# Kernel optimization log

Measured on AMD Instinct MI355X. Metric: run time of the kernel, lower is better.

The kernel has to match this reference:

```python
import jax, jax.numpy as jnp
import numpy as np

B, F = 64, 2048

def setup_inputs() -> dict:
    key = jax.random.key(0)
    k1, k2, k3, k4, k5 = jax.random.split(key, 5)
    scale = 1.0 / np.sqrt(F)
    return {
        "x": jax.random.normal(k1, (B, F), dtype=jnp.float32),
        "feature_mask": jax.random.randint(k2, (B, F), 0, 2, dtype=jnp.int32),
        "Wq": jax.random.normal(k3, (F, F), dtype=jnp.float32) * scale,
        "Wk": jax.random.normal(k4, (F, F), dtype=jnp.float32) * scale,
        "Wv": jax.random.normal(k5, (F, F), dtype=jnp.float32) * scale,
    }

def reference(x, feature_mask, Wq, Wk, Wv):
    # nn.Linear(bias=False): y = x @ W.T
    q = x @ Wq.T  # (B, F)
    k = x @ Wk.T
    v = x @ Wv.T
    # outer-product scores: (B, F, F) = q[:, :, None] * k[:, None, :]
    scores = q[:, :, None] * k[:, None, :]
    # mask broadcast over query dim (unsqueeze(1) in torch)
    scores = jnp.where(feature_mask[:, None, :] == 0, -1e9, scores)
    attn = jax.nn.softmax(scores, axis=-1)  # (B, F, F)
    attended = jnp.einsum("bfg,bg->bf", attn, v)  # (B, F)
    return attended
```

## Files before the change

### kernel.cpp

```cpp
#include <hip/hip_runtime.h>
#include <hip/hip_bf16.h>

#define B 64
#define F 2048
#define BN 32
#define BK 32
#define KSPLIT 4
#define KCHUNK (F / KSPLIT)
#define NITER (KCHUNK / BK)
#define LDSW 40
#define GS 4
#define NSEG 2
#define SEGG 1024

typedef __attribute__((ext_vector_type(8))) short bf16x8;
typedef __attribute__((ext_vector_type(4))) float f32x4;

#define PART_FLOATS (KSPLIT * 3 * B * F)
#define KVC_FLOATS (B * 2 * F)
#define QS_FLOATS (B * F)

#if __has_builtin(__builtin_amdgcn_exp2f)
#define EXP2(x) __builtin_amdgcn_exp2f(x)
#else
#define EXP2(x) exp2f(x)
#endif

__device__ __forceinline__ void split2(float f0, float f1, int& hi, int& lo) {
  union { float f; unsigned u; } a, b;
  a.f = f0; b.f = f1;
  union { unsigned u; float f; } ha, hb;
  ha.u = a.u & 0xFFFF0000u;
  hb.u = b.u & 0xFFFF0000u;
  union { float f; unsigned u; } la, lb;
  la.f = f0 - ha.f;
  lb.f = f1 - hb.f;
  hi = (int)__builtin_amdgcn_perm(b.u, a.u, 0x07060302u);
  lo = (int)__builtin_amdgcn_perm(lb.u, la.u, 0x07060302u);
}

__global__ __launch_bounds__(256) void qkv_gemm_kernel(
    const float* __restrict__ x, const float* __restrict__ Wq,
    const float* __restrict__ Wk, const float* __restrict__ Wv,
    float* __restrict__ part) {
  __shared__ __align__(16) short xs_hi[2][B][LDSW];
  __shared__ __align__(16) short xs_lo[2][B][LDSW];
  __shared__ __align__(16) short ws_hi[2][BN][LDSW];
  __shared__ __align__(16) short ws_lo[2][BN][LDSW];

  const int tid  = threadIdx.x;
  const int f0   = blockIdx.x * BN;
  const int kb   = blockIdx.y;
  const int mat  = blockIdx.z;
  const float* W = (mat == 0) ? Wq : (mat == 1) ? Wk : Wv;

  const int lrow = tid >> 2;
  const int lc0  = (tid & 3) << 3;
  const int wrow = tid >> 3;
  const int wc0  = (tid & 7) << 2;

  const int wave = tid >> 6;
  const int lane = tid & 63;
  const int l15  = lane & 15;
  const int quad = lane >> 4;

  const float* xg = x + lrow * F + kb * KCHUNK + lc0;
  const float* wg = W + (f0 + wrow) * F + kb * KCHUNK + wc0;

  f32x4 acc[2];
#pragma unroll
  for (int i = 0; i < 2; ++i) acc[i] = (f32x4){0.f, 0.f, 0.f, 0.f};

  float4 px[2][2], pw[2];
  px[0][0] = *(const float4*)(xg);
  px[0][1] = *(const float4*)(xg + 4);
  pw[0]    = *(const float4*)(wg);

#pragma unroll
  for (int it = 0; it < NITER; ++it) {
    const int cur = it & 1, nxt = cur ^ 1;
    if (it + 1 < NITER) {
      const float* xp = xg + (it + 1) * BK;
      px[nxt][0] = *(const float4*)(xp);
      px[nxt][1] = *(const float4*)(xp + 4);
      pw[nxt]    = *(const float4*)(wg + (it + 1) * BK);
    }
    int4 xh, xl;
    int2 wh, wl;
    split2(px[cur][0].x, px[cur][0].y, xh.x, xl.x);
    split2(px[cur][0].z, px[cur][0].w, xh.y, xl.y);
    split2(px[cur][1].x, px[cur][1].y, xh.z, xl.z);
    split2(px[cur][1].z, px[cur][1].w, xh.w, xl.w);
    split2(pw[cur].x, pw[cur].y, wh.x, wl.x);
    split2(pw[cur].z, pw[cur].w, wh.y, wl.y);
    *(int4*)&xs_hi[cur][lrow][lc0] = xh;
    *(int4*)&xs_lo[cur][lrow][lc0] = xl;
    *(int2*)&ws_hi[cur][wrow][wc0] = wh;
    *(int2*)&ws_lo[cur][wrow][wc0] = wl;
    __syncthreads();

    bf16x8 a_hi = *(const bf16x8*)&xs_hi[cur][(wave << 4) + l15][quad << 3];
    bf16x8 a_lo = *(const bf16x8*)&xs_lo[cur][(wave << 4) + l15][quad << 3];
#pragma unroll
    for (int nt = 0; nt < 2; ++nt) {
      bf16x8 b_hi = *(const bf16x8*)&ws_hi[cur][(nt << 4) + l15][quad << 3];
      bf16x8 b_lo = *(const bf16x8*)&ws_lo[cur][(nt << 4) + l15][quad << 3];
      acc[nt] = __builtin_amdgcn_mfma_f32_16x16x32_bf16(a_hi, b_hi, acc[nt], 0, 0, 0);
      acc[nt] = __builtin_amdgcn_mfma_f32_16x16x32_bf16(a_hi, b_lo, acc[nt], 0, 0, 0);
      acc[nt] = __builtin_amdgcn_mfma_f32_16x16x32_bf16(a_lo, b_hi, acc[nt], 0, 0, 0);
    }
  }

  float* outp = part + (size_t)(kb * 3 + mat) * B * F;
#pragma unroll
  for (int nt = 0; nt < 2; ++nt) {
    int f = f0 + (nt << 4) + l15;
#pragma unroll
    for (int r = 0; r < 4; ++r) {
      int brow = (wave << 4) + (quad << 2) + r;
      outp[brow * F + f] = acc[nt][r];
    }
  }
}

__global__ __launch_bounds__(256) void prep_kernel(
    const float* __restrict__ part, const int* __restrict__ mask,
    float* __restrict__ kvc, float* __restrict__ qs,
    float* __restrict__ vsum2, float* __restrict__ kmax2,
    float* __restrict__ kmin2, int* __restrict__ cnt2) {
  __shared__ int cnt;
  __shared__ float svs[4], smx[4], smn[4];

  const int b    = blockIdx.x;
  const int seg  = blockIdx.y;
  const int tid  = threadIdx.x;
  const int wave = tid >> 6;
  const int lane = tid & 63;

  if (tid == 0) cnt = 0;
  __syncthreads();

  const int g0 = seg * SEGG + (tid << 2);
  float4 qq = {0.f, 0.f, 0.f, 0.f};
  float4 kq = {0.f, 0.f, 0.f, 0.f}, vq = {0.f, 0.f, 0.f, 0.f};
#pragma unroll
  for (int p = 0; p < KSPLIT; ++p) {
    const float4 qp = *(const float4*)&part[((p * 3 + 0) * B + b) * F + g0];
    const float4 kp = *(const float4*)&part[((p * 3 + 1) * B + b) * F + g0];
    const float4 vp = *(const float4*)&part[((p * 3 + 2) * B + b) * F + g0];
    qq.x += qp.x; qq.y += qp.y; qq.z += qp.z; qq.w += qp.w;
    kq.x += kp.x; kq.y += kp.y; kq.z += kp.z; kq.w += kp.w;
    vq.x += vp.x; vq.y += vp.y; vq.z += vp.z; vq.w += vp.w;
  }
  *(float4*)&qs[b * F + g0] = qq;
  float vs = (vq.x + vq.y) + (vq.z + vq.w);

  const int4 m4 = *(const int4*)&mask[b * F + g0];
  const float kk[4] = {kq.x, kq.y, kq.z, kq.w};
  const float vv[4] = {vq.x, vq.y, vq.z, vq.w};
  const bool  act[4] = {m4.x != 0, m4.y != 0, m4.z != 0, m4.w != 0};

  unsigned long long bal[4];
  int tot = 0;
#pragma unroll
  for (int j = 0; j < 4; ++j) {
    bal[j] = __ballot(act[j]);
    tot += __popcll(bal[j]);
  }
  int base = 0;
  if (lane == 0) base = atomicAdd(&cnt, tot);
  base = __shfl(base, 0);

  float* kvb = kvc + (size_t)b * 2 * F + seg * 2 * SEGG;
  const unsigned long long ltm = (1ull << lane) - 1ull;
  float kmx = -3.4e38f, kmn = 3.4e38f;
  int off = base;
#pragma unroll
  for (int j = 0; j < 4; ++j) {
    if (act[j]) {
      int pos = off + __popcll(bal[j] & ltm);
      *(float2*)&kvb[2 * pos] = (float2){kk[j], vv[j]};
      kmx = fmaxf(kmx, kk[j]);
      kmn = fminf(kmn, kk[j]);
    }
    off += __popcll(bal[j]);
  }

#pragma unroll
  for (int o = 32; o > 0; o >>= 1) {
    vs += __shfl_xor(vs, o);
    kmx = fmaxf(kmx, __shfl_xor(kmx, o));
    kmn = fminf(kmn, __shfl_xor(kmn, o));
  }
  if (lane == 0) { svs[wave] = vs; smx[wave] = kmx; smn[wave] = kmn; }
  __syncthreads();
  if (tid == 0) {
    vsum2[b * NSEG + seg] = svs[0] + svs[1] + svs[2] + svs[3];
    kmax2[b * NSEG + seg] = fmaxf(fmaxf(smx[0], smx[1]), fmaxf(smx[2], smx[3]));
    kmin2[b * NSEG + seg] = fminf(fminf(smn[0], smn[1]), fminf(smn[2], smn[3]));
    cnt2[b * NSEG + seg]  = cnt;
  }
}

__global__ __launch_bounds__(1024, 8) void attn_kernel(
    const float* __restrict__ qs, const float* __restrict__ kvc,
    const float* __restrict__ vsum2, const float* __restrict__ kmax2,
    const float* __restrict__ kmin2, const int* __restrict__ cnt2,
    float* __restrict__ out) {
  __shared__ float rn[GS][256];
  __shared__ float rd[GS][256];

  const int b     = blockIdx.x;
  const int tid   = threadIdx.x;
  const int fl    = tid & 255;
  const int slice = __builtin_amdgcn_readfirstlane(tid >> 8);
  const int fi    = blockIdx.y * 256 + fl;

  const float s = qs[b * F + fi];

  int cnts[NSEG];
  float km = -3.4e38f, kn = 3.4e38f;
  int ntot = 0;
  float vstot = 0.f;
#pragma unroll
  for (int g2 = 0; g2 < NSEG; ++g2) {
    cnts[g2] = cnt2[b * NSEG + g2];
    ntot += cnts[g2];
    km = fmaxf(km, kmax2[b * NSEG + g2]);
    kn = fminf(kn, kmin2[b * NSEG + g2]);
    vstot += vsum2[b * NSEG + g2];
  }

  const float L2E = 1.44269504088896f;
  const float se  = s * L2E;
  const float nm2 = -se * ((s >= 0.f) ? km : kn);

  float n0 = 0.f, n1 = 0.f, n2 = 0.f, n3 = 0.f;
  float d0 = 0.f, d1 = 0.f, d2 = 0.f, d3 = 0.f;
  const float* kvbase = kvc + (size_t)b * 2 * F;
#pragma unroll
  for (int seg = 0; seg < NSEG; ++seg) {
    const int cnt   = cnts[seg];
    const int quads = cnt >> 1;
    const int q0 = (slice * quads) / GS;
    const int q1 = ((slice + 1) * quads) / GS;
    const float4* bp = (const float4*)(kvbase + seg * 2 * SEGG);
    int q = q0;
    for (; q + 4 <= q1; q += 4) {
      float4 p0 = bp[q];
      float4 p1 = bp[q + 1];
      float4 p2 = bp[q + 2];
      float4 p3 = bp[q + 3];
      float e0 = EXP2(fmaf(se, p0.x, nm2));
      float e1 = EXP2(fmaf(se, p0.z, nm2));
      float e2 = EXP2(fmaf(se, p1.x, nm2));
      float e3 = EXP2(fmaf(se, p1.z, nm2));
      float e4 = EXP2(fmaf(se, p2.x, nm2));
      float e5 = EXP2(fmaf(se, p2.z, nm2));
      float e6 = EXP2(fmaf(se, p3.x, nm2));
      float e7 = EXP2(fmaf(se, p3.z, nm2));
      n0 = fmaf(e0, p0.y, n0); d0 += e0;
      n1 = fmaf(e1, p0.w, n1); d1 += e1;
      n2 = fmaf(e2, p1.y, n2); d2 += e2;
      n3 = fmaf(e3, p1.w, n3); d3 += e3;
      n0 = fmaf(e4, p2.y, n0); d0 += e4;
      n1 = fmaf(e5, p2.w, n1); d1 += e5;
      n2 = fmaf(e6, p3.y, n2); d2 += e6;
      n3 = fmaf(e7, p3.w, n3); d3 += e7;
    }
    for (; q < q1; ++q) {
      float4 p0 = bp[q];
      float e0 = EXP2(fmaf(se, p0.x, nm2));
      float e1 = EXP2(fmaf(se, p0.z, nm2));
      n0 = fmaf(e0, p0.y, n0); d0 += e0;
      n1 = fmaf(e1, p0.w, n1); d1 += e1;
    }
    if ((slice == GS - 1) && (cnt & 1)) {
      float2 p = *(const float2*)(kvbase + seg * 2 * SEGG + 2 * (cnt - 1));
      float e = EXP2(fmaf(se, p.x, nm2));
      n2 = fmaf(e, p.y, n2); d2 += e;
    }
  }
  rn[slice][fl] = (n0 + n1) + (n2 + n3);
  rd[slice][fl] = (d0 + d1) + (d2 + d3);
  __syncthreads();
  if (slice == 0) {
    float N = (rn[0][fl] + rn[1][fl]) + (rn[2][fl] + rn[3][fl]);
    float D = (rd[0][fl] + rd[1][fl]) + (rd[2][fl] + rd[3][fl]);
    out[b * F + fi] = (ntot > 0) ? (N / D) : (vstot * (1.0f / (float)F));
  }
}

extern "C" void kernel_launch(void* const* d_in, const int* in_sizes, int n_in,
                              void* d_out, int out_size, void* d_ws, size_t ws_size,
                              hipStream_t stream) {
  const float* x  = (const float*)d_in[0];
  const int* mask = (const int*)d_in[1];
  const float* Wq = (const float*)d_in[2];
  const float* Wk = (const float*)d_in[3];
  const float* Wv = (const float*)d_in[4];
  float* out = (float*)d_out;

  float* part  = (float*)d_ws;
  float* kvc   = part + PART_FLOATS;
  float* qs    = kvc + KVC_FLOATS;
  float* vsum2 = qs + QS_FLOATS;
  float* kmx2  = vsum2 + B * NSEG;
  float* kmn2  = kmx2 + B * NSEG;
  int*   cnt2  = (int*)(kmn2 + B * NSEG);

  dim3 gg(F / BN, KSPLIT, 3);
  qkv_gemm_kernel<<<gg, 256, 0, stream>>>(x, Wq, Wk, Wv, part);
  dim3 gp(B, NSEG);
  prep_kernel<<<gp, 256, 0, stream>>>(part, mask, kvc, qs, vsum2, kmx2, kmn2, cnt2);
  dim3 ga(B, F / 256);
  attn_kernel<<<ga, 1024, 0, stream>>>(qs, kvc, vsum2, kmx2, kmn2, cnt2, out);
}
```

Baseline: 122.6 us.

## Fuse prep into attention kernel, compacting masked keys into LDS per block

Removes the separate prep kernel. Each attention block now reduces the split-K partials for its own q values and for the full k/v row, then compacts unmasked (k,v) pairs into shared memory via ballot and atomics. The block also computes max/min of k and the sum of v. The inner softmax loop reads from LDS instead of global memory, and one launch plus the global intermediates go away. In exchange, each of the 8 blocks per batch row redoes the k/v reduction and compaction, and each block uses about 16KB of extra LDS, which may lower occupancy.

```diff
diff --git a/kernel.cpp b/kernel.cpp
--- a/kernel.cpp
+++ b/kernel.cpp
@@ -10,15 +10,11 @@
 #define NITER (KCHUNK / BK)
 #define LDSW 40
 #define GS 4
-#define NSEG 2
-#define SEGG 1024
 
 typedef __attribute__((ext_vector_type(8))) short bf16x8;
 typedef __attribute__((ext_vector_type(4))) float f32x4;
 
 #define PART_FLOATS (KSPLIT * 3 * B * F)
-#define KVC_FLOATS (B * 2 * F)
-#define QS_FLOATS (B * F)
 
 #if __has_builtin(__builtin_amdgcn_exp2f)
 #define EXP2(x) __builtin_amdgcn_exp2f(x)
@@ -123,112 +119,79 @@
   }
 }
 
-__global__ __launch_bounds__(256) void prep_kernel(
+__global__ __launch_bounds__(1024, 8) void attn_kernel(
     const float* __restrict__ part, const int* __restrict__ mask,
-    float* __restrict__ kvc, float* __restrict__ qs,
-    float* __restrict__ vsum2, float* __restrict__ kmax2,
-    float* __restrict__ kmin2, int* __restrict__ cnt2) {
-  __shared__ int cnt;
-  __shared__ float svs[4], smx[4], smn[4];
-
-  const int b    = blockIdx.x;
-  const int seg  = blockIdx.y;
-  const int tid  = threadIdx.x;
-  const int wave = tid >> 6;
-  const int lane = tid & 63;
-
-  if (tid == 0) cnt = 0;
-  __syncthreads();
-
-  const int g0 = seg * SEGG + (tid << 2);
-  float4 qq = {0.f, 0.f, 0.f, 0.f};
-  float4 kq = {0.f, 0.f, 0.f, 0.f}, vq = {0.f, 0.f, 0.f, 0.f};
-#pragma unroll
-  for (int p = 0; p < KSPLIT; ++p) {
-    const float4 qp = *(const float4*)&part[((p * 3 + 0) * B + b) * F + g0];
-    const float4 kp = *(const float4*)&part[((p * 3 + 1) * B + b) * F + g0];
-    const float4 vp = *(const float4*)&part[((p * 3 + 2) * B + b) * F + g0];
-    qq.x += qp.x; qq.y += qp.y; qq.z += qp.z; qq.w += qp.w;
-    kq.x += kp.x; kq.y += kp.y; kq.z += kp.z; kq.w += kp.w;
-    vq.x += vp.x; vq.y += vp.y; vq.z += vp.z; vq.w += vp.w;
-  }
-  *(float4*)&qs[b * F + g0] = qq;
-  float vs = (vq.x + vq.y) + (vq.z + vq.w);
-
-  const int4 m4 = *(const int4*)&mask[b * F + g0];
-  const float kk[4] = {kq.x, kq.y, kq.z, kq.w};
-  const float vv[4] = {vq.x, vq.y, vq.z, vq.w};
-  const bool  act[4] = {m4.x != 0, m4.y != 0, m4.z != 0, m4.w != 0};
-
-  unsigned long long bal[4];
-  int tot = 0;
-#pragma unroll
-  for (int j = 0; j < 4; ++j) {
-    bal[j] = __ballot(act[j]);
-    tot += __popcll(bal[j]);
-  }
-  int base = 0;
-  if (lane == 0) base = atomicAdd(&cnt, tot);
-  base = __shfl(base, 0);
-
-  float* kvb = kvc + (size_t)b * 2 * F + seg * 2 * SEGG;
-  const unsigned long long ltm = (1ull << lane) - 1ull;
-  float kmx = -3.4e38f, kmn = 3.4e38f;
-  int off = base;
-#pragma unroll
-  for (int j = 0; j < 4; ++j) {
-    if (act[j]) {
-      int pos = off + __popcll(bal[j] & ltm);
-      *(float2*)&kvb[2 * pos] = (float2){kk[j], vv[j]};
-      kmx = fmaxf(kmx, kk[j]);
-      kmn = fminf(kmn, kk[j]);
-    }
-    off += __popcll(bal[j]);
-  }
-
-#pragma unroll
-  for (int o = 32; o > 0; o >>= 1) {
-    vs += __shfl_xor(vs, o);
-    kmx = fmaxf(kmx, __shfl_xor(kmx, o));
-    kmn = fminf(kmn, __shfl_xor(kmn, o));
-  }
-  if (lane == 0) { svs[wave] = vs; smx[wave] = kmx; smn[wave] = kmn; }
-  __syncthreads();
-  if (tid == 0) {
-    vsum2[b * NSEG + seg] = svs[0] + svs[1] + svs[2] + svs[3];
-    kmax2[b * NSEG + seg] = fmaxf(fmaxf(smx[0], smx[1]), fmaxf(smx[2], smx[3]));
-    kmin2[b * NSEG + seg] = fminf(fminf(smn[0], smn[1]), fminf(smn[2], smn[3]));
-    cnt2[b * NSEG + seg]  = cnt;
-  }
-}
-
-__global__ __launch_bounds__(1024, 8) void attn_kernel(
-    const float* __restrict__ qs, const float* __restrict__ kvc,
-    const float* __restrict__ vsum2, const float* __restrict__ kmax2,
-    const float* __restrict__ kmin2, const int* __restrict__ cnt2,
     float* __restrict__ out) {
+  __shared__ __align__(16) float kvs[2 * F];
   __shared__ float rn[GS][256];
   __shared__ float rd[GS][256];
+  __shared__ float swv[16], swm[16], swn[16];
+  __shared__ int scnt;
 
   const int b     = blockIdx.x;
   const int tid   = threadIdx.x;
   const int fl    = tid & 255;
   const int slice = __builtin_amdgcn_readfirstlane(tid >> 8);
   const int fi    = blockIdx.y * 256 + fl;
-
-  const float s = qs[b * F + fi];
-
-  int cnts[NSEG];
-  float km = -3.4e38f, kn = 3.4e38f;
-  int ntot = 0;
-  float vstot = 0.f;
-#pragma unroll
-  for (int g2 = 0; g2 < NSEG; ++g2) {
-    cnts[g2] = cnt2[b * NSEG + g2];
-    ntot += cnts[g2];
-    km = fmaxf(km, kmax2[b * NSEG + g2]);
-    kn = fminf(kn, kmin2[b * NSEG + g2]);
-    vstot += vsum2[b * NSEG + g2];
+  const int wid   = tid >> 6;
+  const int lane  = tid & 63;
+
+  if (tid == 0) scnt = 0;
+  __syncthreads();
+
+  float s = 0.f;
+#pragma unroll
+  for (int p = 0; p < KSPLIT; ++p) s += part[((p * 3 + 0) * B + b) * F + fi];
+
+  const int g0 = tid << 1;
+  float2 k2 = {0.f, 0.f}, v2 = {0.f, 0.f};
+#pragma unroll
+  for (int p = 0; p < KSPLIT; ++p) {
+    const float2 kp = *(const float2*)&part[((p * 3 + 1) * B + b) * F + g0];
+    const float2 vp = *(const float2*)&part[((p * 3 + 2) * B + b) * F + g0];
+    k2.x += kp.x; k2.y += kp.y;
+    v2.x += vp.x; v2.y += vp.y;
+  }
+  float vs = v2.x + v2.y;
+
+  const int2 m2 = *(const int2*)&mask[b * F + g0];
+  const bool a0 = (m2.x != 0), a1 = (m2.y != 0);
+  const unsigned long long bal0 = __ballot(a0);
+  const unsigned long long bal1 = __ballot(a1);
+  const int tot = __popcll(bal0) + __popcll(bal1);
+  int base = 0;
+  if (lane == 0) base = atomicAdd(&scnt, tot);
+  base = __shfl(base, 0);
+
+  const unsigned long long ltm = (1ull << lane) - 1ull;
+  float kmx = -3.4e38f, kmn = 3.4e38f;
+  if (a0) {
+    int pos = base + __popcll(bal0 & ltm);
+    *(float2*)&kvs[2 * pos] = (float2){k2.x, v2.x};
+    kmx = fmaxf(kmx, k2.x); kmn = fminf(kmn, k2.x);
+  }
+  if (a1) {
+    int pos = base + __popcll(bal0) + __popcll(bal1 & ltm);
+    *(float2*)&kvs[2 * pos] = (float2){k2.y, v2.y};
+    kmx = fmaxf(kmx, k2.y); kmn = fminf(kmn, k2.y);
+  }
+
+#pragma unroll
+  for (int o = 32; o > 0; o >>= 1) {
+    vs += __shfl_xor(vs, o);
+    kmx = fmaxf(kmx, __shfl_xor(kmx, o));
+    kmn = fminf(kmn, __shfl_xor(kmn, o));
+  }
+  if (lane == 0) { swv[wid] = vs; swm[wid] = kmx; swn[wid] = kmn; }
+  __syncthreads();
+
+  const int ntot = scnt;
+  float km = -3.4e38f, kn = 3.4e38f, vstot = 0.f;
+#pragma unroll
+  for (int w = 0; w < 16; ++w) {
+    km = fmaxf(km, swm[w]);
+    kn = fminf(kn, swn[w]);
+    vstot += swv[w];
   }
 
   const float L2E = 1.44269504088896f;
@@ -237,14 +200,11 @@
 
   float n0 = 0.f, n1 = 0.f, n2 = 0.f, n3 = 0.f;
   float d0 = 0.f, d1 = 0.f, d2 = 0.f, d3 = 0.f;
-  const float* kvbase = kvc + (size_t)b * 2 * F;
-#pragma unroll
-  for (int seg = 0; seg < NSEG; ++seg) {
-    const int cnt   = cnts[seg];
-    const int quads = cnt >> 1;
+  {
+    const int quads = ntot >> 1;
     const int q0 = (slice * quads) / GS;
     const int q1 = ((slice + 1) * quads) / GS;
-    const float4* bp = (const float4*)(kvbase + seg * 2 * SEGG);
+    const float4* bp = (const float4*)kvs;
     int q = q0;
     for (; q + 4 <= q1; q += 4) {
       float4 p0 = bp[q];
@@ -275,8 +235,8 @@
       n0 = fmaf(e0, p0.y, n0); d0 += e0;
       n1 = fmaf(e1, p0.w, n1); d1 += e1;
     }
-    if ((slice == GS - 1) && (cnt & 1)) {
-      float2 p = *(const float2*)(kvbase + seg * 2 * SEGG + 2 * (cnt - 1));
+    if ((slice == GS - 1) && (ntot & 1)) {
+      float2 p = *(const float2*)(kvs + 2 * (ntot - 1));
       float e = EXP2(fmaf(se, p.x, nm2));
       n2 = fmaf(e, p.y, n2); d2 += e;
     }
@@ -301,18 +261,10 @@
   const float* Wv = (const float*)d_in[4];
   float* out = (float*)d_out;
 
-  float* part  = (float*)d_ws;
-  float* kvc   = part + PART_FLOATS;
-  float* qs    = kvc + KVC_FLOATS;
-  float* vsum2 = qs + QS_FLOATS;
-  float* kmx2  = vsum2 + B * NSEG;
-  float* kmn2  = kmx2 + B * NSEG;
-  int*   cnt2  = (int*)(kmn2 + B * NSEG);
+  float* part = (float*)d_ws;
 
   dim3 gg(F / BN, KSPLIT, 3);
   qkv_gemm_kernel<<<gg, 256, 0, stream>>>(x, Wq, Wk, Wv, part);
-  dim3 gp(B, NSEG);
-  prep_kernel<<<gp, 256, 0, stream>>>(part, mask, kvc, qs, vsum2, kmx2, kmn2, cnt2);
   dim3 ga(B, F / 256);
-  attn_kernel<<<ga, 1024, 0, stream>>>(qs, kvc, vsum2, kmx2, kmn2, cnt2, out);
-}
+  attn_kernel<<<ga, 1024, 0, stream>>>(part, mask, out);
+}
```

Measured after the change: 121.2 us. Within noise of the previous version (-1.2%).
